# Performance work log

Measured on AMD Instinct MI355X. Metric: run time of the kernel, lower is better.

## Reference

```python
import jax, jax.numpy as jnp
import numpy as np

NHEAD = 8
HEAD_DIM = 64
HIDDEN = 512
ROPE_BASE = 10000.0


def _rope_cos_sin(L, dim, dtype):
    inv_freq = 1.0 / (ROPE_BASE ** (jnp.arange(0, dim, 2, dtype=jnp.float32) / dim))
    t = jnp.arange(L, dtype=jnp.float32)
    freqs = jnp.outer(t, inv_freq)                # [L, dim/2]
    emb = jnp.concatenate([freqs, freqs], axis=-1)  # [L, dim]
    return jnp.cos(emb).astype(dtype), jnp.sin(emb).astype(dtype)


def _rotate_half(x):
    x1, x2 = jnp.split(x, 2, axis=-1)
    return jnp.concatenate([-x2, x1], axis=-1)


def setup_inputs() -> dict:
    key = jax.random.key(0)
    ks = jax.random.split(key, 5)
    B, L = 8, 1024
    scale = 0.02
    return {
        "x": jax.random.normal(ks[0], (B, L, HIDDEN), dtype=jnp.float32),
        "Wq": jax.random.normal(ks[1], (HIDDEN, HIDDEN), dtype=jnp.float32) * scale,
        "Wk": jax.random.normal(ks[2], (HIDDEN, HIDDEN), dtype=jnp.float32) * scale,
        "Wv": jax.random.normal(ks[3], (HIDDEN, HIDDEN), dtype=jnp.float32) * scale,
        "Wo": jax.random.normal(ks[4], (HIDDEN, HIDDEN), dtype=jnp.float32) * scale,
    }


def reference(x, Wq, Wk, Wv, Wo):
    B, L, _ = x.shape
    # QKV projections (nn.Linear stores weight as [out, in]; y = x @ W.T)
    def proj(W):
        y = jnp.einsum('bld,ed->ble', x, W)
        return y.reshape(B, L, NHEAD, HEAD_DIM).transpose(0, 2, 1, 3)  # [B,H,L,Dh]
    q, k, v = proj(Wq), proj(Wk), proj(Wv)

    cos, sin = _rope_cos_sin(L, HEAD_DIM, x.dtype)   # [L, Dh]
    cos = cos[None, None]                            # [1,1,L,Dh]
    sin = sin[None, None]
    q = q * cos + _rotate_half(q) * sin
    k = k * cos + _rotate_half(k) * sin

    # scaled dot-product attention (no mask, eval mode -> dropout 0)
    scores = jnp.einsum('bhqd,bhkd->bhqk', q, k) / jnp.sqrt(jnp.asarray(HEAD_DIM, x.dtype))
    attn = jax.nn.softmax(scores, axis=-1)
    out = jnp.einsum('bhqk,bhkd->bhqd', attn, v)     # [B,H,L,Dh]
    out = out.transpose(0, 2, 1, 3).reshape(B, L, HIDDEN)
    return jnp.einsum('ble,oe->blo', out, Wo)
```

## Files before the change

kernel.cpp:

```cpp
#include <hip/hip_runtime.h>
#include <math.h>


#define BB 8
#define LL 1024
#define HH 8
#define DH 64
#define HID 512

typedef __bf16 bf16x8 __attribute__((ext_vector_type(8)));
typedef float f32x4 __attribute__((ext_vector_type(4)));
typedef unsigned short u16x8 __attribute__((ext_vector_type(8)));
typedef unsigned short u16x4 __attribute__((ext_vector_type(4)));

__device__ inline unsigned short f2bf(float f) {
    union { float f; unsigned u; } v; v.f = f;
    unsigned r = v.u + 0x7fffu + ((v.u >> 16) & 1u);
    return (unsigned short)(r >> 16);
}
__device__ inline float bf2f(unsigned short s) {
    union { unsigned u; float f; } v; v.u = ((unsigned)s) << 16;
    return v.f;
}

#define GLOAD_LDS16(g, l) __builtin_amdgcn_global_load_lds( \
    (const __attribute__((address_space(1))) unsigned int*)(g), \
    (__attribute__((address_space(3))) unsigned int*)(l), 16, 0, 0)

__global__ __launch_bounds__(256) void convert_kernel(
    const float* __restrict__ x, const float* __restrict__ Wq,
    const float* __restrict__ Wk, const float* __restrict__ Wv,
    const float* __restrict__ Wo,
    unsigned short* __restrict__ xb, unsigned short* __restrict__ wqb,
    unsigned short* __restrict__ wkb, unsigned short* __restrict__ wvb,
    unsigned short* __restrict__ wob,
    float* __restrict__ cos_t, float* __restrict__ sin_t)
{
    int blk = blockIdx.x;
    if (blk >= 2560) {
        int idx = (blk - 2560) * 256 + threadIdx.x;
        int l = idx >> 5, j = idx & 31;
        float inv = exp2f(-(float)j * (13.287712379549449f / 32.0f));
        float th = (float)l * inv;
        cos_t[idx] = cosf(th);
        sin_t[idx] = sinf(th);
        return;
    }
    const float* s; unsigned short* d; int off;
    if (blk < 2048) { s = x; d = xb; off = blk; }
    else {
        int t = (blk - 2048) >> 7;
        off = (blk - 2048) & 127;
        s = (t == 0) ? Wq : (t == 1) ? Wk : (t == 2) ? Wv : Wo;
        d = (t == 0) ? wqb : (t == 1) ? wkb : (t == 2) ? wvb : wob;
    }
    size_t base = ((size_t)off * 256 + threadIdx.x) * 8;
    float4 a = *(const float4*)(s + base);
    float4 b = *(const float4*)(s + base + 4);
    u16x8 pk;
    pk[0] = f2bf(a.x); pk[1] = f2bf(a.y); pk[2] = f2bf(a.z); pk[3] = f2bf(a.w);
    pk[4] = f2bf(b.x); pk[5] = f2bf(b.y); pk[6] = f2bf(b.z); pk[7] = f2bf(b.w);
    *(u16x8*)(d + base) = pk;
}

__global__ __launch_bounds__(256) void qkv_gemm_kernel(
    const unsigned short* __restrict__ xb, const unsigned short* __restrict__ Wqb,
    const unsigned short* __restrict__ Wkb, const unsigned short* __restrict__ Wvb,
    const float* __restrict__ cos_t, const float* __restrict__ sin_t,
    unsigned short* __restrict__ Qb, unsigned short* __restrict__ Kb,
    unsigned short* __restrict__ Vt)
{
    __shared__ unsigned short As[128 * 32];
    __shared__ unsigned short Bs[128 * 32];

    const int mt = blockIdx.x;
    const int nt = blockIdx.y;
    const int mbase = mt * 128;
    const int mat = nt >> 2;
    const unsigned short* W = (mat == 0) ? Wqb : ((mat == 1) ? Wkb : Wvb);
    const int nW = (nt & 3) * 128;

    const int tid = threadIdx.x;
    const int w = tid >> 6, lane = tid & 63;
    const int wr = w >> 1, wc = w & 1;
    const int l15 = lane & 15, koff = (lane >> 4) * 8;
    const int srow = (lane >> 2);
    const int scol = (lane & 3) * 8;

    f32x4 acc[4][4];
    #pragma unroll
    for (int i = 0; i < 4; ++i)
        #pragma unroll
        for (int j = 0; j < 4; ++j) acc[i][j] = (f32x4){0.f, 0.f, 0.f, 0.f};

    for (int kc = 0; kc < 512; kc += 32) {
        __syncthreads();
        #pragma unroll
        for (int j = 0; j < 2; ++j) {
            int row = w * 32 + j * 16;
            GLOAD_LDS16(xb + (size_t)(mbase + row + srow) * 512 + kc + scol,
                        As + row * 32);
            GLOAD_LDS16(W + (size_t)(nW + row + srow) * 512 + kc + scol,
                        Bs + row * 32);
        }
        __syncthreads();

        bf16x8 af[4], bf[4];
        #pragma unroll
        for (int mi = 0; mi < 4; ++mi)
            af[mi] = *(const bf16x8*)&As[(wr * 64 + mi * 16 + l15) * 32 + koff];
        #pragma unroll
        for (int ni = 0; ni < 4; ++ni)
            bf[ni] = *(const bf16x8*)&Bs[(wc * 64 + ni * 16 + l15) * 32 + koff];
        #pragma unroll
        for (int mi = 0; mi < 4; ++mi)
            #pragma unroll
            for (int ni = 0; ni < 4; ++ni)
                acc[mi][ni] = __builtin_amdgcn_mfma_f32_16x16x32_bf16(
                    af[mi], bf[ni], acc[mi][ni], 0, 0, 0);
    }

    const int h = (nt & 3) * 2 + wc;
    if (mat < 2) {
        unsigned short* D = (mat == 0) ? Qb : Kb;
        const float sc = (mat == 0) ? 0.18033688011112042f  : 1.0f;
        #pragma unroll
        for (int mi = 0; mi < 4; ++mi) {
            int m = mbase + wr * 64 + mi * 16 + (lane >> 4) * 4;
            int b = m >> 10, l0 = m & 1023;
            #pragma unroll
            for (int r = 0; r < 4; ++r) {
                int l = l0 + r;
                float c0 = cos_t[l * 32 + l15],      s0 = sin_t[l * 32 + l15];
                float c1 = cos_t[l * 32 + 16 + l15], s1 = sin_t[l * 32 + 16 + l15];
                float a0 = acc[mi][0][r], a1 = acc[mi][1][r];
                float a2 = acc[mi][2][r], a3 = acc[mi][3][r];
                float o0 = (a0 * c0 - a2 * s0) * sc;
                float o1 = (a1 * c1 - a3 * s1) * sc;
                float o2 = (a2 * c0 + a0 * s0) * sc;
                float o3 = (a3 * c1 + a1 * s1) * sc;
                size_t rowbase = ((size_t)(b * HH + h) * LL + l) * 64;
                D[rowbase +  0 + l15] = f2bf(o0);
                D[rowbase + 16 + l15] = f2bf(o1);
                D[rowbase + 32 + l15] = f2bf(o2);
                D[rowbase + 48 + l15] = f2bf(o3);
            }
        }
    } else {
        #pragma unroll
        for (int mi = 0; mi < 4; ++mi) {
            int m = mbase + wr * 64 + mi * 16 + (lane >> 4) * 4;
            int b = m >> 10, l0 = m & 1023;
            #pragma unroll
            for (int ni = 0; ni < 4; ++ni) {
                int d = ni * 16 + l15;
                u16x4 pk;
                #pragma unroll
                for (int r = 0; r < 4; ++r) pk[r] = f2bf(acc[mi][ni][r]);
                *(u16x4*)(Vt + ((size_t)(b * HH + h) * 64 + d) * LL + l0) = pk;
            }
        }
    }
}

__global__ __launch_bounds__(256) void attn_kernel(
    const unsigned short* __restrict__ Q, const unsigned short* __restrict__ K,
    const unsigned short* __restrict__ Vt, unsigned short* __restrict__ O)
{
    __shared__ unsigned short Ks[2][64 * 64];
    __shared__ unsigned short Vs[2][64 * 64];
    __shared__ unsigned short Plds[4][32][72];

    const int wgid = blockIdx.x;
    const int xcd = wgid & 7;
    const int j = wgid >> 3;
    const int bh = xcd * 8 + (j >> 3);
    const int qt = j & 7;
    const int b = bh >> 3, h = bh & 7;
    const int tid = threadIdx.x;
    const int w = tid >> 6;
    const int lane = tid & 63;
    const int l15 = lane & 15;
    const int g4 = (lane >> 4) * 4;
    const int koff = (lane >> 4) * 8;

    const unsigned short* Qp = Q + (size_t)bh * LL * 64;
    const unsigned short* Kp = K + (size_t)bh * LL * 64;
    const unsigned short* Vp = Vt + (size_t)bh * 64 * LL;

    const int sr0 = (0 * 4 + w) * 8 + (lane >> 3);
    const int sr1 = (1 * 4 + w) * 8 + (lane >> 3);
    const int scsw = ((lane & 7) * 8) ^ (((lane >> 3) & 7) * 8);
    const int sd0 = (0 * 4 + w) * 512;
    const int sd1 = (1 * 4 + w) * 512;

    const int q0 = qt * 128 + w * 32;

    bf16x8 qfA0 = *(const bf16x8*)(Qp + (size_t)(q0 + l15) * 64 + koff);
    bf16x8 qfA1 = *(const bf16x8*)(Qp + (size_t)(q0 + l15) * 64 + koff + 32);
    bf16x8 qfB0 = *(const bf16x8*)(Qp + (size_t)(q0 + 16 + l15) * 64 + koff);
    bf16x8 qfB1 = *(const bf16x8*)(Qp + (size_t)(q0 + 16 + l15) * 64 + koff + 32);

    float lsumA = 0.f, lsumB = 0.f;
    f32x4 opvA[4], opvB[4];
    #pragma unroll
    for (int dt = 0; dt < 4; ++dt) {
        opvA[dt] = (f32x4){0.f, 0.f, 0.f, 0.f};
        opvB[dt] = (f32x4){0.f, 0.f, 0.f, 0.f};
    }

    GLOAD_LDS16(Kp + (size_t)sr0 * 64 + scsw, &Ks[0][sd0]);
    GLOAD_LDS16(Kp + (size_t)sr1 * 64 + scsw, &Ks[0][sd1]);
    GLOAD_LDS16(Vp + (size_t)sr0 * LL + scsw, &Vs[0][sd0]);
    GLOAD_LDS16(Vp + (size_t)sr1 * LL + scsw, &Vs[0][sd1]);
    __syncthreads();

    for (int kt = 0; kt < 16; ++kt) {
        const int cur = kt & 1, nxt = cur ^ 1;
        const int kbase = kt * 64;

        if (kt < 15) {
            GLOAD_LDS16(Kp + (size_t)(kbase + 64 + sr0) * 64 + scsw, &Ks[nxt][sd0]);
            GLOAD_LDS16(Kp + (size_t)(kbase + 64 + sr1) * 64 + scsw, &Ks[nxt][sd1]);
            GLOAD_LDS16(Vp + (size_t)sr0 * LL + kbase + 64 + scsw, &Vs[nxt][sd0]);
            GLOAD_LDS16(Vp + (size_t)sr1 * LL + kbase + 64 + scsw, &Vs[nxt][sd1]);
        }

        f32x4 sA[4], sB[4];
        __builtin_amdgcn_s_setprio(1);
        #pragma unroll
        for (int nt = 0; nt < 4; ++nt) {
            int row = nt * 16 + l15;
            int off  = row * 64 + (koff ^ ((row & 7) * 8));
            int off1 = row * 64 + ((koff + 32) ^ ((row & 7) * 8));
            bf16x8 kf0 = *(const bf16x8*)&Ks[cur][off];
            bf16x8 kf1 = *(const bf16x8*)&Ks[cur][off1];
            f32x4 zA = {0.f, 0.f, 0.f, 0.f};
            zA = __builtin_amdgcn_mfma_f32_16x16x32_bf16(kf0, qfA0, zA, 0, 0, 0);
            zA = __builtin_amdgcn_mfma_f32_16x16x32_bf16(kf1, qfA1, zA, 0, 0, 0);
            sA[nt] = zA;
            f32x4 zB = {0.f, 0.f, 0.f, 0.f};
            zB = __builtin_amdgcn_mfma_f32_16x16x32_bf16(kf0, qfB0, zB, 0, 0, 0);
            zB = __builtin_amdgcn_mfma_f32_16x16x32_bf16(kf1, qfB1, zB, 0, 0, 0);
            sB[nt] = zB;
        }
        __builtin_amdgcn_s_setprio(0);

        #pragma unroll
        for (int nt = 0; nt < 4; ++nt) {
            float p0 = exp2f(sA[nt][0]);
            float p1 = exp2f(sA[nt][1]);
            float p2 = exp2f(sA[nt][2]);
            float p3 = exp2f(sA[nt][3]);
            lsumA += (p0 + p1) + (p2 + p3);
            unsigned d0, d1;
            asm("v_cvt_pk_bf16_f32 %0, %1, %2" : "=v"(d0) : "v"(p0), "v"(p1));
            asm("v_cvt_pk_bf16_f32 %0, %1, %2" : "=v"(d1) : "v"(p2), "v"(p3));
            unsigned long long pk = ((unsigned long long)d1 << 32) | d0;
            *(unsigned long long*)&Plds[w][l15][nt * 16 + g4] = pk;
        }
        #pragma unroll
        for (int nt = 0; nt < 4; ++nt) {
            float p0 = exp2f(sB[nt][0]);
            float p1 = exp2f(sB[nt][1]);
            float p2 = exp2f(sB[nt][2]);
            float p3 = exp2f(sB[nt][3]);
            lsumB += (p0 + p1) + (p2 + p3);
            unsigned d0, d1;
            asm("v_cvt_pk_bf16_f32 %0, %1, %2" : "=v"(d0) : "v"(p0), "v"(p1));
            asm("v_cvt_pk_bf16_f32 %0, %1, %2" : "=v"(d1) : "v"(p2), "v"(p3));
            unsigned long long pk = ((unsigned long long)d1 << 32) | d0;
            *(unsigned long long*)&Plds[w][16 + l15][nt * 16 + g4] = pk;
        }

        bf16x8 pfA0 = *(const bf16x8*)&Plds[w][l15][koff];
        bf16x8 pfA1 = *(const bf16x8*)&Plds[w][l15][koff + 32];
        bf16x8 pfB0 = *(const bf16x8*)&Plds[w][16 + l15][koff];
        bf16x8 pfB1 = *(const bf16x8*)&Plds[w][16 + l15][koff + 32];

        __builtin_amdgcn_s_setprio(1);
        #pragma unroll
        for (int dt = 0; dt < 4; ++dt) {
            int row = dt * 16 + l15;
            int off  = row * 64 + (koff ^ ((row & 7) * 8));
            int off1 = row * 64 + ((koff + 32) ^ ((row & 7) * 8));
            bf16x8 vf0 = *(const bf16x8*)&Vs[cur][off];
            bf16x8 vf1 = *(const bf16x8*)&Vs[cur][off1];
            opvA[dt] = __builtin_amdgcn_mfma_f32_16x16x32_bf16(vf0, pfA0, opvA[dt], 0, 0, 0);
            opvA[dt] = __builtin_amdgcn_mfma_f32_16x16x32_bf16(vf1, pfA1, opvA[dt], 0, 0, 0);
            opvB[dt] = __builtin_amdgcn_mfma_f32_16x16x32_bf16(vf0, pfB0, opvB[dt], 0, 0, 0);
            opvB[dt] = __builtin_amdgcn_mfma_f32_16x16x32_bf16(vf1, pfB1, opvB[dt], 0, 0, 0);
        }
        __builtin_amdgcn_s_setprio(0);

        __syncthreads();
    }

    lsumA += __shfl_xor(lsumA, 16);
    lsumA += __shfl_xor(lsumA, 32);
    lsumB += __shfl_xor(lsumB, 16);
    lsumB += __shfl_xor(lsumB, 32);

    const float invA = 1.f / lsumA;
    const float invB = 1.f / lsumB;
    const int lA = q0 + l15, lB = q0 + 16 + l15;
    #pragma unroll
    for (int dt = 0; dt < 4; ++dt) {
        u16x4 pkA, pkB;
        #pragma unroll
        for (int r = 0; r < 4; ++r) {
            pkA[r] = f2bf(opvA[dt][r] * invA);
            pkB[r] = f2bf(opvB[dt][r] * invB);
        }
        *(u16x4*)(O + (size_t)(b * LL + lA) * HID + h * 64 + dt * 16 + g4) = pkA;
        *(u16x4*)(O + (size_t)(b * LL + lB) * HID + h * 64 + dt * 16 + g4) = pkB;
    }
}

__global__ __launch_bounds__(256) void out_gemm_kernel(
    const unsigned short* __restrict__ AOb, const unsigned short* __restrict__ Wob,
    float* __restrict__ out)
{
    __shared__ unsigned short As[128 * 32];
    __shared__ unsigned short Bs[64 * 32];

    const int mt = blockIdx.x;
    const int nt = blockIdx.y;
    const int mbase = mt * 128;
    const int nbase = nt * 64;

    const int tid = threadIdx.x;
    const int w = tid >> 6, lane = tid & 63;
    const int wr = w >> 1, wc = w & 1;
    const int l15 = lane & 15, koff = (lane >> 4) * 8;
    const int srow = (lane >> 2);
    const int scol = (lane & 3) * 8;
    const int br = (lane >> 3);
    const int bc = (lane & 7) * 8;

    f32x4 acc[4][2];
    #pragma unroll
    for (int i = 0; i < 4; ++i)
        #pragma unroll
        for (int j = 0; j < 2; ++j) acc[i][j] = (f32x4){0.f, 0.f, 0.f, 0.f};

    for (int kc = 0; kc < 512; kc += 32) {
        __syncthreads();
        #pragma unroll
        for (int j = 0; j < 2; ++j) {
            int row = w * 32 + j * 16;
            GLOAD_LDS16(AOb + (size_t)(mbase + row + srow) * 512 + kc + scol,
                        As + row * 32);
        }
        {
            int row = w * 16 + srow;
            GLOAD_LDS16(Wob + (size_t)(nbase + row) * 512 + kc + scol,
                        Bs + (w * 16) * 32);
        }
        __syncthreads();

        bf16x8 af[4], bf[2];
        #pragma unroll
        for (int mi = 0; mi < 4; ++mi)
            af[mi] = *(const bf16x8*)&As[(wr * 64 + mi * 16 + l15) * 32 + koff];
        #pragma unroll
        for (int ni = 0; ni < 2; ++ni)
            bf[ni] = *(const bf16x8*)&Bs[(wc * 32 + ni * 16 + l15) * 32 + koff];
        #pragma unroll
        for (int mi = 0; mi < 4; ++mi)
            #pragma unroll
            for (int ni = 0; ni < 2; ++ni)
                acc[mi][ni] = __builtin_amdgcn_mfma_f32_16x16x32_bf16(
                    af[mi], bf[ni], acc[mi][ni], 0, 0, 0);
    }

    #pragma unroll
    for (int mi = 0; mi < 4; ++mi) {
        int m = mbase + wr * 64 + mi * 16 + (lane >> 4) * 4;
        #pragma unroll
        for (int r = 0; r < 4; ++r) {
            size_t rowbase = (size_t)(m + r) * 512 + nbase + wc * 32;
            #pragma unroll
            for (int ni = 0; ni < 2; ++ni)
                out[rowbase + ni * 16 + l15] = acc[mi][ni][r];
        }
    }
}

extern "C" void kernel_launch(void* const* d_in, const int* in_sizes, int n_in,
                              void* d_out, int out_size, void* d_ws, size_t ws_size,
                              hipStream_t stream) {
    const float* x  = (const float*)d_in[0];
    const float* Wq = (const float*)d_in[1];
    const float* Wk = (const float*)d_in[2];
    const float* Wv = (const float*)d_in[3];
    const float* Wo = (const float*)d_in[4];
    float* out = (float*)d_out;

    const size_t tblN = (size_t)LL * 32;
    const size_t qkvN = (size_t)BB * HH * LL * 64;
    const size_t wN   = (size_t)HID * HID;

    float* cos_t = (float*)d_ws;
    float* sin_t = cos_t + tblN;
    unsigned short* Qb  = (unsigned short*)(sin_t + tblN);
    unsigned short* Kb  = Qb + qkvN;
    unsigned short* Vt  = Kb + qkvN;
    unsigned short* xb  = Vt + qkvN;
    unsigned short* Wqb = xb + qkvN;
    unsigned short* Wkb = Wqb + wN;
    unsigned short* Wvb = Wkb + wN;
    unsigned short* Wob = Wvb + wN;
    unsigned short* AOb = Wob + wN;

    hipLaunchKernelGGL(convert_kernel, dim3(2048 + 512 + 128), dim3(256), 0, stream,
                       x, Wq, Wk, Wv, Wo, xb, Wqb, Wkb, Wvb, Wob, cos_t, sin_t);
    hipLaunchKernelGGL(qkv_gemm_kernel, dim3(64, 12), dim3(256), 0, stream,
                       xb, Wqb, Wkb, Wvb, cos_t, sin_t, Qb, Kb, Vt);
    hipLaunchKernelGGL(attn_kernel, dim3(512), dim3(256), 0, stream,
                       Qb, Kb, Vt, AOb);
    hipLaunchKernelGGL(out_gemm_kernel, dim3(64, 8), dim3(256), 0, stream,
                       AOb, Wob, out);
}
```

Measured before the change: 86.78 us.

## Switch attention to 32x32x16 MFMA and keep P in registers via permlane swap

```diff
diff --git a/kernel.cpp b/kernel.cpp
--- a/kernel.cpp
+++ b/kernel.cpp
@@ -10,22 +10,35 @@
 
 typedef __bf16 bf16x8 __attribute__((ext_vector_type(8)));
 typedef float f32x4 __attribute__((ext_vector_type(4)));
+typedef float f32x16 __attribute__((ext_vector_type(16)));
 typedef unsigned short u16x8 __attribute__((ext_vector_type(8)));
 typedef unsigned short u16x4 __attribute__((ext_vector_type(4)));
+typedef unsigned u32x4 __attribute__((ext_vector_type(4)));
 
 __device__ inline unsigned short f2bf(float f) {
     union { float f; unsigned u; } v; v.f = f;
     unsigned r = v.u + 0x7fffu + ((v.u >> 16) & 1u);
     return (unsigned short)(r >> 16);
 }
-__device__ inline float bf2f(unsigned short s) {
-    union { unsigned u; float f; } v; v.u = ((unsigned)s) << 16;
-    return v.f;
-}
 
 #define GLOAD_LDS16(g, l) __builtin_amdgcn_global_load_lds( \
     (const __attribute__((address_space(1))) unsigned int*)(g), \
     (__attribute__((address_space(3))) unsigned int*)(l), 16, 0, 0)
+
+__device__ inline bf16x8 pack8(float e0, float e1, float e2, float e3,
+                               float e4, float e5, float e6, float e7) {
+    unsigned a0, a1, a2, a3;
+    asm("v_cvt_pk_bf16_f32 %0, %1, %2" : "=v"(a0) : "v"(e0), "v"(e1));
+    asm("v_cvt_pk_bf16_f32 %0, %1, %2" : "=v"(a1) : "v"(e2), "v"(e3));
+    asm("v_cvt_pk_bf16_f32 %0, %1, %2" : "=v"(a2) : "v"(e4), "v"(e5));
+    asm("v_cvt_pk_bf16_f32 %0, %1, %2" : "=v"(a3) : "v"(e6), "v"(e7));
+    asm("v_permlane32_swap_b32 %0, %1" : "+v"(a0), "+v"(a2));
+    asm("v_permlane32_swap_b32 %0, %1" : "+v"(a1), "+v"(a3));
+    u32x4 wv; wv[0] = a0; wv[1] = a1; wv[2] = a2; wv[3] = a3;
+    return *(bf16x8*)&wv;
+}
+
+#define Z16 {0.f,0.f,0.f,0.f,0.f,0.f,0.f,0.f,0.f,0.f,0.f,0.f,0.f,0.f,0.f,0.f}
 
 __global__ __launch_bounds__(256) void convert_kernel(
     const float* __restrict__ x, const float* __restrict__ Wq,
@@ -169,7 +182,6 @@
 {
     __shared__ unsigned short Ks[2][64 * 64];
     __shared__ unsigned short Vs[2][64 * 64];
-    __shared__ unsigned short Plds[4][32][72];
 
     const int wgid = blockIdx.x;
     const int xcd = wgid & 7;
@@ -180,34 +192,36 @@
     const int tid = threadIdx.x;
     const int w = tid >> 6;
     const int lane = tid & 63;
-    const int l15 = lane & 15;
-    const int g4 = (lane >> 4) * 4;
-    const int koff = (lane >> 4) * 8;
+    const int l31 = lane & 31;
+    const int hi5 = lane >> 5;
 
     const unsigned short* Qp = Q + (size_t)bh * LL * 64;
     const unsigned short* Kp = K + (size_t)bh * LL * 64;
     const unsigned short* Vp = Vt + (size_t)bh * 64 * LL;
 
-    const int sr0 = (0 * 4 + w) * 8 + (lane >> 3);
-    const int sr1 = (1 * 4 + w) * 8 + (lane >> 3);
+    const int sr0 = w * 8 + (lane >> 3);
+    const int sr1 = 32 + w * 8 + (lane >> 3);
     const int scsw = ((lane & 7) * 8) ^ (((lane >> 3) & 7) * 8);
-    const int sd0 = (0 * 4 + w) * 512;
-    const int sd1 = (1 * 4 + w) * 512;
+    const int sd0 = w * 512;
+    const int sd1 = 2048 + w * 512;
 
     const int q0 = qt * 128 + w * 32;
 
-    bf16x8 qfA0 = *(const bf16x8*)(Qp + (size_t)(q0 + l15) * 64 + koff);
-    bf16x8 qfA1 = *(const bf16x8*)(Qp + (size_t)(q0 + l15) * 64 + koff + 32);
-    bf16x8 qfB0 = *(const bf16x8*)(Qp + (size_t)(q0 + 16 + l15) * 64 + koff);
-    bf16x8 qfB1 = *(const bf16x8*)(Qp + (size_t)(q0 + 16 + l15) * 64 + koff + 32);
-
-    float lsumA = 0.f, lsumB = 0.f;
-    f32x4 opvA[4], opvB[4];
-    #pragma unroll
-    for (int dt = 0; dt < 4; ++dt) {
-        opvA[dt] = (f32x4){0.f, 0.f, 0.f, 0.f};
-        opvB[dt] = (f32x4){0.f, 0.f, 0.f, 0.f};
-    }
+    bf16x8 qf0 = *(const bf16x8*)(Qp + (size_t)(q0 + l31) * 64 +  0 + hi5 * 8);
+    bf16x8 qf1 = *(const bf16x8*)(Qp + (size_t)(q0 + l31) * 64 + 16 + hi5 * 8);
+    bf16x8 qf2 = *(const bf16x8*)(Qp + (size_t)(q0 + l31) * 64 + 32 + hi5 * 8);
+    bf16x8 qf3 = *(const bf16x8*)(Qp + (size_t)(q0 + l31) * 64 + 48 + hi5 * 8);
+
+    const int swz = (l31 & 7) * 8;
+    const int co0 = ( 0 + hi5 * 8) ^ swz;
+    const int co1 = (16 + hi5 * 8) ^ swz;
+    const int co2 = (32 + hi5 * 8) ^ swz;
+    const int co3 = (48 + hi5 * 8) ^ swz;
+    const int rA = l31 * 64;
+    const int rB = (32 + l31) * 64;
+
+    float lsum = 0.f;
+    f32x16 opv0 = Z16, opv1 = Z16;
 
     GLOAD_LDS16(Kp + (size_t)sr0 * 64 + scsw, &Ks[0][sd0]);
     GLOAD_LDS16(Kp + (size_t)sr1 * 64 + scsw, &Ks[0][sd1]);
@@ -226,94 +240,82 @@
             GLOAD_LDS16(Vp + (size_t)sr1 * LL + kbase + 64 + scsw, &Vs[nxt][sd1]);
         }
 
-        f32x4 sA[4], sB[4];
+        f32x16 s0 = Z16, s1 = Z16;
         __builtin_amdgcn_s_setprio(1);
-        #pragma unroll
-        for (int nt = 0; nt < 4; ++nt) {
-            int row = nt * 16 + l15;
-            int off  = row * 64 + (koff ^ ((row & 7) * 8));
-            int off1 = row * 64 + ((koff + 32) ^ ((row & 7) * 8));
-            bf16x8 kf0 = *(const bf16x8*)&Ks[cur][off];
-            bf16x8 kf1 = *(const bf16x8*)&Ks[cur][off1];
-            f32x4 zA = {0.f, 0.f, 0.f, 0.f};
-            zA = __builtin_amdgcn_mfma_f32_16x16x32_bf16(kf0, qfA0, zA, 0, 0, 0);
-            zA = __builtin_amdgcn_mfma_f32_16x16x32_bf16(kf1, qfA1, zA, 0, 0, 0);
-            sA[nt] = zA;
-            f32x4 zB = {0.f, 0.f, 0.f, 0.f};
-            zB = __builtin_amdgcn_mfma_f32_16x16x32_bf16(kf0, qfB0, zB, 0, 0, 0);
-            zB = __builtin_amdgcn_mfma_f32_16x16x32_bf16(kf1, qfB1, zB, 0, 0, 0);
-            sB[nt] = zB;
+        {
+            bf16x8 kA, kB;
+            kA = *(const bf16x8*)&Ks[cur][rA + co0];
+            kB = *(const bf16x8*)&Ks[cur][rB + co0];
+            s0 = __builtin_amdgcn_mfma_f32_32x32x16_bf16(kA, qf0, s0, 0, 0, 0);
+            s1 = __builtin_amdgcn_mfma_f32_32x32x16_bf16(kB, qf0, s1, 0, 0, 0);
+            kA = *(const bf16x8*)&Ks[cur][rA + co1];
+            kB = *(const bf16x8*)&Ks[cur][rB + co1];
+            s0 = __builtin_amdgcn_mfma_f32_32x32x16_bf16(kA, qf1, s0, 0, 0, 0);
+            s1 = __builtin_amdgcn_mfma_f32_32x32x16_bf16(kB, qf1, s1, 0, 0, 0);
+            kA = *(const bf16x8*)&Ks[cur][rA + co2];
+            kB = *(const bf16x8*)&Ks[cur][rB + co2];
+            s0 = __builtin_amdgcn_mfma_f32_32x32x16_bf16(kA, qf2, s0, 0, 0, 0);
+            s1 = __builtin_amdgcn_mfma_f32_32x32x16_bf16(kB, qf2, s1, 0, 0, 0);
+            kA = *(const bf16x8*)&Ks[cur][rA + co3];
+            kB = *(const bf16x8*)&Ks[cur][rB + co3];
+            s0 = __builtin_amdgcn_mfma_f32_32x32x16_bf16(kA, qf3, s0, 0, 0, 0);
+            s1 = __builtin_amdgcn_mfma_f32_32x32x16_bf16(kB, qf3, s1, 0, 0, 0);
         }
         __builtin_amdgcn_s_setprio(0);
 
-        #pragma unroll
-        for (int nt = 0; nt < 4; ++nt) {
-            float p0 = exp2f(sA[nt][0]);
-            float p1 = exp2f(sA[nt][1]);
-            float p2 = exp2f(sA[nt][2]);
-            float p3 = exp2f(sA[nt][3]);
-            lsumA += (p0 + p1) + (p2 + p3);
-            unsigned d0, d1;
-            asm("v_cvt_pk_bf16_f32 %0, %1, %2" : "=v"(d0) : "v"(p0), "v"(p1));
-            asm("v_cvt_pk_bf16_f32 %0, %1, %2" : "=v"(d1) : "v"(p2), "v"(p3));
-            unsigned long long pk = ((unsigned long long)d1 << 32) | d0;
-            *(unsigned long long*)&Plds[w][l15][nt * 16 + g4] = pk;
-        }
-        #pragma unroll
-        for (int nt = 0; nt < 4; ++nt) {
-            float p0 = exp2f(sB[nt][0]);
-            float p1 = exp2f(sB[nt][1]);
-            float p2 = exp2f(sB[nt][2]);
-            float p3 = exp2f(sB[nt][3]);
-            lsumB += (p0 + p1) + (p2 + p3);
-            unsigned d0, d1;
-            asm("v_cvt_pk_bf16_f32 %0, %1, %2" : "=v"(d0) : "v"(p0), "v"(p1));
-            asm("v_cvt_pk_bf16_f32 %0, %1, %2" : "=v"(d1) : "v"(p2), "v"(p3));
-            unsigned long long pk = ((unsigned long long)d1 << 32) | d0;
-            *(unsigned long long*)&Plds[w][16 + l15][nt * 16 + g4] = pk;
-        }
-
-        bf16x8 pfA0 = *(const bf16x8*)&Plds[w][l15][koff];
-        bf16x8 pfA1 = *(const bf16x8*)&Plds[w][l15][koff + 32];
-        bf16x8 pfB0 = *(const bf16x8*)&Plds[w][16 + l15][koff];
-        bf16x8 pfB1 = *(const bf16x8*)&Plds[w][16 + l15][koff + 32];
+        float e[16], f[16];
+        #pragma unroll
+        for (int i = 0; i < 16; ++i) e[i] = exp2f(s0[i]);
+        #pragma unroll
+        for (int i = 0; i < 16; ++i) f[i] = exp2f(s1[i]);
+        lsum += (((e[0]+e[1])+(e[2]+e[3])) + ((e[4]+e[5])+(e[6]+e[7])))
+              + (((e[8]+e[9])+(e[10]+e[11])) + ((e[12]+e[13])+(e[14]+e[15])));
+        lsum += (((f[0]+f[1])+(f[2]+f[3])) + ((f[4]+f[5])+(f[6]+f[7])))
+              + (((f[8]+f[9])+(f[10]+f[11])) + ((f[12]+f[13])+(f[14]+f[15])));
+        bf16x8 pf0 = pack8(e[0], e[1], e[2], e[3], e[4], e[5], e[6], e[7]);
+        bf16x8 pf1 = pack8(e[8], e[9], e[10], e[11], e[12], e[13], e[14], e[15]);
+        bf16x8 pf2 = pack8(f[0], f[1], f[2], f[3], f[4], f[5], f[6], f[7]);
+        bf16x8 pf3 = pack8(f[8], f[9], f[10], f[11], f[12], f[13], f[14], f[15]);
 
         __builtin_amdgcn_s_setprio(1);
-        #pragma unroll
-        for (int dt = 0; dt < 4; ++dt) {
-            int row = dt * 16 + l15;
-            int off  = row * 64 + (koff ^ ((row & 7) * 8));
-            int off1 = row * 64 + ((koff + 32) ^ ((row & 7) * 8));
-            bf16x8 vf0 = *(const bf16x8*)&Vs[cur][off];
-            bf16x8 vf1 = *(const bf16x8*)&Vs[cur][off1];
-            opvA[dt] = __builtin_amdgcn_mfma_f32_16x16x32_bf16(vf0, pfA0, opvA[dt], 0, 0, 0);
-            opvA[dt] = __builtin_amdgcn_mfma_f32_16x16x32_bf16(vf1, pfA1, opvA[dt], 0, 0, 0);
-            opvB[dt] = __builtin_amdgcn_mfma_f32_16x16x32_bf16(vf0, pfB0, opvB[dt], 0, 0, 0);
-            opvB[dt] = __builtin_amdgcn_mfma_f32_16x16x32_bf16(vf1, pfB1, opvB[dt], 0, 0, 0);
+        {
+            bf16x8 vA, vB;
+            vA = *(const bf16x8*)&Vs[cur][rA + co0];
+            vB = *(const bf16x8*)&Vs[cur][rB + co0];
+            opv0 = __builtin_amdgcn_mfma_f32_32x32x16_bf16(vA, pf0, opv0, 0, 0, 0);
+            opv1 = __builtin_amdgcn_mfma_f32_32x32x16_bf16(vB, pf0, opv1, 0, 0, 0);
+            vA = *(const bf16x8*)&Vs[cur][rA + co1];
+            vB = *(const bf16x8*)&Vs[cur][rB + co1];
+            opv0 = __builtin_amdgcn_mfma_f32_32x32x16_bf16(vA, pf1, opv0, 0, 0, 0);
+            opv1 = __builtin_amdgcn_mfma_f32_32x32x16_bf16(vB, pf1, opv1, 0, 0, 0);
+            vA = *(const bf16x8*)&Vs[cur][rA + co2];
+            vB = *(const bf16x8*)&Vs[cur][rB + co2];
+            opv0 = __builtin_amdgcn_mfma_f32_32x32x16_bf16(vA, pf2, opv0, 0, 0, 0);
+            opv1 = __builtin_amdgcn_mfma_f32_32x32x16_bf16(vB, pf2, opv1, 0, 0, 0);
+            vA = *(const bf16x8*)&Vs[cur][rA + co3];
+            vB = *(const bf16x8*)&Vs[cur][rB + co3];
+            opv0 = __builtin_amdgcn_mfma_f32_32x32x16_bf16(vA, pf3, opv0, 0, 0, 0);
+            opv1 = __builtin_amdgcn_mfma_f32_32x32x16_bf16(vB, pf3, opv1, 0, 0, 0);
         }
         __builtin_amdgcn_s_setprio(0);
 
         __syncthreads();
     }
 
-    lsumA += __shfl_xor(lsumA, 16);
-    lsumA += __shfl_xor(lsumA, 32);
-    lsumB += __shfl_xor(lsumB, 16);
-    lsumB += __shfl_xor(lsumB, 32);
-
-    const float invA = 1.f / lsumA;
-    const float invB = 1.f / lsumB;
-    const int lA = q0 + l15, lB = q0 + 16 + l15;
+    lsum += __shfl_xor(lsum, 32);
+
+    const float inv = 1.f / lsum;
+    unsigned short* ob = O + (size_t)(b * LL + q0 + l31) * HID + h * 64;
     #pragma unroll
-    for (int dt = 0; dt < 4; ++dt) {
+    for (int rg = 0; rg < 4; ++rg) {
         u16x4 pkA, pkB;
         #pragma unroll
-        for (int r = 0; r < 4; ++r) {
-            pkA[r] = f2bf(opvA[dt][r] * invA);
-            pkB[r] = f2bf(opvB[dt][r] * invB);
-        }
-        *(u16x4*)(O + (size_t)(b * LL + lA) * HID + h * 64 + dt * 16 + g4) = pkA;
-        *(u16x4*)(O + (size_t)(b * LL + lB) * HID + h * 64 + dt * 16 + g4) = pkB;
+        for (int rr = 0; rr < 4; ++rr) {
+            pkA[rr] = f2bf(opv0[rg * 4 + rr] * inv);
+            pkB[rr] = f2bf(opv1[rg * 4 + rr] * inv);
+        }
+        *(u16x4*)(ob + rg * 8 + hi5 * 4)      = pkA;
+        *(u16x4*)(ob + 32 + rg * 8 + hi5 * 4) = pkB;
     }
 }
 
@@ -335,8 +337,6 @@
     const int l15 = lane & 15, koff = (lane >> 4) * 8;
     const int srow = (lane >> 2);
     const int scol = (lane & 3) * 8;
-    const int br = (lane >> 3);
-    const int bc = (lane & 7) * 8;
 
     f32x4 acc[4][2];
     #pragma unroll
```

Result: faster. 83.64 us (-3.6%).
